# Performance work log

Hardware: AMD Instinct MI355X
Metric: run time of the kernel (lower is better)

The kernel has to match this reference:

```python
import jax, jax.numpy as jnp
import numpy as np

N = 20000      # total nodes
E = 160000     # total edges
NG = 128       # graphs in batch
POS_DIM = 48   # pos_embedding_dim
CTX = 128      # context_vector_dim
TYP = 80       # types_embedding_dim
HID = 256      # hidden_dim = POS_DIM + CTX + TYP
H = 4          # heads
C = HID        # per-head channels (concat=False)
OUT = 1024
L = 3
EF = 5
EPS_BN = 1e-5


def setup_inputs() -> dict:
    key = jax.random.key(0)
    ks = jax.random.split(key, 16)
    s = 0.02
    return {
        "x_types": jax.random.randint(ks[0], (N,), 0, 118),
        "pos": jax.random.normal(ks[1], (N, 3)) * 5.0,
        "edge_index": jax.random.randint(ks[2], (2, E), 0, N),
        "edge_attr": jax.random.uniform(ks[3], (E, EF)),
        "batch": jnp.sort(jax.random.randint(ks[4], (N,), 0, NG)),
        "context_vector": jax.random.normal(ks[5], (NG, CTX)),
        "emb_W": jax.random.normal(ks[6], (118, TYP)) * s,
        "emb_b": jnp.zeros((TYP,)),
        "lin_W": jax.random.normal(ks[7], (L, HID, H * C)) * s,
        "att_src": jax.random.normal(ks[8], (L, H, C)) * s,
        "att_dst": jax.random.normal(ks[9], (L, H, C)) * s,
        "edge_W": jax.random.normal(ks[10], (L, EF, H * C)) * s,
        "att_edge": jax.random.normal(ks[11], (L, H, C)) * s,
        "conv_b": jnp.zeros((L, C)),
        "bn_gamma": jnp.ones((L, C)),
        "bn_beta": jnp.zeros((L, C)),
        "out_W": jax.random.normal(ks[12], (HID, OUT)) * s,
        "out_b": jnp.zeros((OUT,)),
    }


def sinusoidal_pe(pos, dim):
    # per-coordinate [sin, cos] blocks, coords concatenated in x,y,z order
    half = dim // 2
    cdim = dim // 3
    div = jnp.exp(jnp.arange(half, dtype=pos.dtype) * (-jnp.log(jnp.asarray(10000.0, pos.dtype)) / half))[: cdim // 2]
    s = pos[:, :, None] * div                       # [N, 3, cdim//2]
    emb = jnp.concatenate([jnp.sin(s), jnp.cos(s)], axis=-1)  # [N, 3, cdim]
    return emb.reshape(pos.shape[0], dim)


def gat_layer(x, src, dst, eattr, W, a_s, a_d, eW, a_e, b):
    n = x.shape[0]
    xl = (x @ W).reshape(n, H, C)                   # [N,H,C]
    a_src = jnp.einsum('nhc,hc->nh', xl, a_s)[src]  # [E,H]
    a_dst = jnp.einsum('nhc,hc->nh', xl, a_d)[dst]
    ee = (eattr @ eW).reshape(-1, H, C)             # [E,H,C]
    a_edge = jnp.einsum('ehc,hc->eh', ee, a_e)
    alpha = jax.nn.leaky_relu(a_src + a_dst + a_edge, negative_slope=0.2)  # [E,H]
    amax = jax.ops.segment_max(alpha, dst, num_segments=n)
    ex = jnp.exp(alpha - jnp.where(jnp.isfinite(amax), amax, 0.0)[dst])
    denom = jax.ops.segment_sum(ex, dst, num_segments=n)
    w = ex / (denom[dst] + 1e-16)                   # segment softmax over incoming edges
    msg = xl[src] * w[..., None]                    # [E,H,C]
    out = jax.ops.segment_sum(msg, dst, num_segments=n)  # [N,H,C]
    return out.mean(axis=1) + b                     # concat=False -> head mean


def reference(x_types, pos, edge_index, edge_attr, batch, context_vector,
              emb_W, emb_b, lin_W, att_src, att_dst, edge_W, att_edge,
              conv_b, bn_gamma, bn_beta, out_W, out_b):
    types = jax.nn.one_hot(x_types, 118, dtype=emb_W.dtype)
    te = types @ emb_W + emb_b
    pe = sinusoidal_pe(pos, POS_DIM)
    x = jnp.concatenate([te, pe, context_vector[batch]], axis=1)  # [N, HID]
    src, dst = edge_index[0], edge_index[1]
    for l in range(L):
        xc = gat_layer(x, src, dst, edge_attr, lin_W[l], att_src[l],
                       att_dst[l], edge_W[l], att_edge[l], conv_b[l])
        mu = xc.mean(axis=0)
        var = xc.var(axis=0)
        xc = (xc - mu) / jnp.sqrt(var + EPS_BN) * bn_gamma[l] + bn_beta[l]
        xc = jax.nn.gelu(xc, approximate=False)
        x = x + xc                                   # residual ('res')
    x = x @ out_W + out_b                            # [N, OUT]
    return jax.ops.segment_sum(x, batch, num_segments=NG)  # global_add_pool
```

## Files before the change

kernel.cpp:

```cpp
#include <hip/hip_runtime.h>
#include <hip/hip_bf16.h>
#include <math.h>

#define N_NODES 20000
#define N_EDGES 160000
#define NGRAPH  128
#define NLAYER  3
#define M_PAD   20096

typedef short bf16x8 __attribute__((ext_vector_type(8)));
typedef float f32x4  __attribute__((ext_vector_type(4)));

__device__ __forceinline__ ushort f2bf(float x) {
    __hip_bfloat16 h = __float2bfloat16(x);
    return *(ushort*)&h;
}
__device__ __forceinline__ float bf2f(ushort u) {
    __hip_bfloat16 h = *(__hip_bfloat16*)&u;
    return __bfloat162float(h);
}

__device__ __forceinline__ void gload16(const void* g, void* l) {
    __builtin_amdgcn_global_load_lds(
        (const __attribute__((address_space(1))) void*)g,
        (__attribute__((address_space(3))) void*)l, 16, 0, 0);
}

__global__ __launch_bounds__(256) void k_node_init(
    const int* __restrict__ xt, const float* __restrict__ pos,
    const int* __restrict__ batch, const float* __restrict__ ctx,
    const float* __restrict__ embW, const float* __restrict__ embb,
    float* __restrict__ x)
{
    int n = blockIdx.x;
    int c = threadIdx.x;
    float v;
    if (c < 80) {
        v = embW[xt[n] * 80 + c] + embb[c];
    } else if (c < 128) {
        int j = c - 80;
        int coord = j >> 4;
        int k = j & 15;
        float p = pos[n * 3 + coord];
        int i = (k < 8) ? k : (k - 8);
        float factor = -logf(10000.0f) / 24.0f;
        float d = expf(factor * (float)i);
        float s = p * d;
        v = (k < 8) ? sinf(s) : cosf(s);
    } else {
        v = ctx[batch[n] * 128 + (c - 128)];
    }
    x[n * 256 + c] = v;
}

__global__ __launch_bounds__(256) void k_prepW(
    const float* __restrict__ W, ushort* __restrict__ Bthi, ushort* __restrict__ Btlo)
{
    int idx = blockIdx.x * 256 + threadIdx.x;
    int c   = idx & 255;
    int kap = idx >> 8;
    int k = kap & 255, h = kap >> 8;
    float w = W[(size_t)k * 1024 + h * 256 + c];
    ushort hi = f2bf(w);
    ushort lo = f2bf(w - bf2f(hi));
    int pos = c * 1024 + (kap ^ ((c & 3) << 3));
    Bthi[pos] = hi;
    Btlo[pos] = lo;
}

__global__ __launch_bounds__(256) void k_gemm_mfma(
    const ushort* __restrict__ Ahi, const ushort* __restrict__ Alo,
    const ushort* __restrict__ Bhi, const ushort* __restrict__ Blo,
    const float* __restrict__ convb, float* __restrict__ xc, int M)
{
    __shared__ ushort sAh[64 * 32];
    __shared__ ushort sAl[64 * 32];
    __shared__ ushort sBh[128 * 32];
    __shared__ ushort sBl[128 * 32];

    const int tid  = threadIdx.x;
    const int lane = tid & 63;
    const int wv   = tid >> 6;
    const int wr   = (wv >> 1) * 32;
    const int wc   = (wv & 1) * 64;
    const int bm   = blockIdx.y * 64;
    const int bn   = blockIdx.x * 128;
    const int r15  = lane & 15;
    const int g    = lane >> 4;

    f32x4 acc[2][4] = {};

    for (int kt = 0; kt < 1024; kt += 32) {
        {
            int row = tid >> 2, ch = tid & 3;
            size_t ga = (size_t)(bm + row) * 1024 + kt + ch * 8;
            uint la = (uint)tid * 16;
            gload16(&Ahi[ga], (char*)sAh + la);
            gload16(&Alo[ga], (char*)sAl + la);
        }
#pragma unroll
        for (int call = 0; call < 2; ++call) {
            int i   = call * 256 + tid;
            int row = i >> 2, ch = i & 3;
            size_t gb = (size_t)(bn + row) * 1024 + kt + ch * 8;
            uint lb = (uint)i * 16;
            gload16(&Bhi[gb], (char*)sBh + lb);
            gload16(&Blo[gb], (char*)sBl + lb);
        }
        __syncthreads();

        bf16x8 afh[2], afl[2], bfh[4], bfl[4];
#pragma unroll
        for (int f = 0; f < 2; ++f) {
            int rowA = wr + f * 16 + r15;
            int offA = rowA * 64 + ((g << 4) ^ ((rowA & 3) << 4));
            afh[f] = *(const bf16x8*)((const char*)sAh + offA);
            afl[f] = *(const bf16x8*)((const char*)sAl + offA);
        }
#pragma unroll
        for (int f = 0; f < 4; ++f) {
            int rowB = wc + f * 16 + r15;
            int offB = rowB * 64 + ((g << 4) ^ ((rowB & 3) << 4));
            bfh[f] = *(const bf16x8*)((const char*)sBh + offB);
            bfl[f] = *(const bf16x8*)((const char*)sBl + offB);
        }
#pragma unroll
        for (int fi = 0; fi < 2; ++fi)
#pragma unroll
            for (int fj = 0; fj < 4; ++fj) {
                acc[fi][fj] = __builtin_amdgcn_mfma_f32_16x16x32_bf16(
                    afh[fi], bfh[fj], acc[fi][fj], 0, 0, 0);
                acc[fi][fj] = __builtin_amdgcn_mfma_f32_16x16x32_bf16(
                    afh[fi], bfl[fj], acc[fi][fj], 0, 0, 0);
                acc[fi][fj] = __builtin_amdgcn_mfma_f32_16x16x32_bf16(
                    afl[fi], bfh[fj], acc[fi][fj], 0, 0, 0);
            }
        __syncthreads();
    }

#pragma unroll
    for (int fi = 0; fi < 2; ++fi) {
#pragma unroll
        for (int fj = 0; fj < 4; ++fj) {
#pragma unroll
            for (int r = 0; r < 4; ++r) {
                int row = bm + wr + fi * 16 + g * 4 + r;
                int col = bn + wc + fj * 16 + r15;
                if (row < M)
                    xc[(size_t)row * 256 + col] = 0.25f * acc[fi][fj][r] + convb[col];
            }
        }
    }
}

__global__ __launch_bounds__(256) void k_uvec(
    const float* __restrict__ W, const float* __restrict__ aS,
    const float* __restrict__ aD, float* __restrict__ uS, float* __restrict__ uD)
{
    int wid  = blockIdx.x * 4 + (threadIdx.x >> 6);
    int lane = threadIdx.x & 63;
    int h = wid >> 8;
    int k = wid & 255;
    float4 w = *(const float4*)&W[(size_t)k * 1024 + h * 256 + lane * 4];
    float4 s = *(const float4*)&aS[h * 256 + lane * 4];
    float4 d = *(const float4*)&aD[h * 256 + lane * 4];
    float ps = w.x * s.x + w.y * s.y + w.z * s.z + w.w * s.w;
    float pd = w.x * d.x + w.y * d.y + w.z * d.z + w.w * d.w;
    for (int o = 32; o; o >>= 1) {
        ps += __shfl_down(ps, o, 64);
        pd += __shfl_down(pd, o, 64);
    }
    if (lane == 0) { uS[h * 256 + k] = ps; uD[h * 256 + k] = pd; }
}

__global__ __launch_bounds__(256) void k_attn_dots_x(
    const float* __restrict__ x, const float* __restrict__ uS,
    const float* __restrict__ uD, float* __restrict__ asrc, float* __restrict__ adst)
{
    int n = blockIdx.x;
    int h = threadIdx.x >> 6;
    int lane = threadIdx.x & 63;
    float4 xv = *(const float4*)&x[(size_t)n * 256 + lane * 4];
    float4 sv = *(const float4*)&uS[h * 256 + lane * 4];
    float4 dv = *(const float4*)&uD[h * 256 + lane * 4];
    float ps = xv.x * sv.x + xv.y * sv.y + xv.z * sv.z + xv.w * sv.w;
    float pd = xv.x * dv.x + xv.y * dv.y + xv.z * dv.z + xv.w * dv.w;
    for (int o = 32; o; o >>= 1) {
        ps += __shfl_down(ps, o, 64);
        pd += __shfl_down(pd, o, 64);
    }
    if (lane == 0) { asrc[n * 4 + h] = ps; adst[n * 4 + h] = pd; }
}

__global__ void k_edge_M(const float* __restrict__ eW, const float* __restrict__ aE,
                         float* __restrict__ M)
{
    int f = blockIdx.x >> 2, h = blockIdx.x & 3;
    int lane = threadIdx.x;
    float4 w = *(const float4*)&eW[f * 1024 + h * 256 + lane * 4];
    float4 a = *(const float4*)&aE[h * 256 + lane * 4];
    float p = w.x * a.x + w.y * a.y + w.z * a.z + w.w * a.w;
    for (int o = 32; o; o >>= 1) p += __shfl_down(p, o, 64);
    if (lane == 0) M[f * 4 + h] = p;
}

__global__ __launch_bounds__(256) void k_edge_alpha(
    const int* __restrict__ src, const int* __restrict__ dst,
    const float* __restrict__ ea, const float* __restrict__ asrc,
    const float* __restrict__ adst, const float* __restrict__ M,
    const int* __restrict__ pos, float* __restrict__ ex)
{
    int e = blockIdx.x * 256 + threadIdx.x;
    if (e >= N_EDGES) return;
    int s = src[e], d = dst[e];
    float as_[4], ad_[4];
    *(float4*)as_ = *(const float4*)&asrc[s * 4];
    *(float4*)ad_ = *(const float4*)&adst[d * 4];
    float f[5];
#pragma unroll
    for (int i = 0; i < 5; ++i) f[i] = ea[e * 5 + i];
    float r[4];
#pragma unroll
    for (int h = 0; h < 4; ++h) {
        float m = f[0]*M[h] + f[1]*M[4+h] + f[2]*M[8+h] + f[3]*M[12+h] + f[4]*M[16+h];
        float al = as_[h] + ad_[h] + m;
        al = (al >= 0.f) ? al : 0.2f * al;
        r[h] = expf(al);
    }
    *(float4*)&ex[(size_t)pos[e] * 4] = *(float4*)r;
}

__global__ void k_hist(const int* __restrict__ dst, int* __restrict__ deg)
{
    int e = blockIdx.x * 256 + threadIdx.x;
    if (e < N_EDGES) atomicAdd(&deg[dst[e]], 1);
}

#define SCAN_T 1024
__global__ __launch_bounds__(1024) void k_scan(
    const int* __restrict__ deg, int* __restrict__ off, int* __restrict__ cursor)
{
    __shared__ int sums[SCAN_T];
    int t = threadIdx.x;
    const int CHK = (N_NODES + SCAN_T - 1) / SCAN_T;
    int base = t * CHK;
    int s = 0;
    for (int i = 0; i < CHK; ++i) {
        int idx = base + i;
        if (idx < N_NODES) s += deg[idx];
    }
    sums[t] = s;
    __syncthreads();
    for (int o = 1; o < SCAN_T; o <<= 1) {
        int v = (t >= o) ? sums[t - o] : 0;
        __syncthreads();
        sums[t] += v;
        __syncthreads();
    }
    int run = (t > 0) ? sums[t - 1] : 0;
    for (int i = 0; i < CHK; ++i) {
        int idx = base + i;
        if (idx < N_NODES) {
            off[idx] = run; cursor[idx] = run;
            run += deg[idx];
        }
    }
    if (t == SCAN_T - 1) off[N_NODES] = sums[SCAN_T - 1];
}

__global__ void k_scatter(const int* __restrict__ dst, const int* __restrict__ src,
                          int* __restrict__ cursor, int* __restrict__ pos,
                          int* __restrict__ srcs)
{
    int e = blockIdx.x * 256 + threadIdx.x;
    if (e >= N_EDGES) return;
    int p = atomicAdd(&cursor[dst[e]], 1);
    pos[e] = p;
    srcs[p] = src[e];
}

__global__ __launch_bounds__(256) void k_aggregate_x(
    const float* __restrict__ x, const float* __restrict__ ex,
    const int* __restrict__ off, const int* __restrict__ srcs,
    ushort* __restrict__ agghi, ushort* __restrict__ agglo)
{
    int n = blockIdx.x;
    int c = threadIdx.x;
    int e0 = off[n], e1 = off[n + 1];
    float a0 = 0.f, a1 = 0.f, a2 = 0.f, a3 = 0.f;
    float d0 = 0.f, d1 = 0.f, d2 = 0.f, d3 = 0.f;
    for (int e = e0; e < e1; ++e) {
        float4 w = *(const float4*)&ex[(size_t)e * 4];
        float xv = x[(size_t)srcs[e] * 256 + c];
        a0 += w.x * xv; a1 += w.y * xv; a2 += w.z * xv; a3 += w.w * xv;
        d0 += w.x; d1 += w.y; d2 += w.z; d3 += w.w;
    }
    float v[4];
    v[0] = a0 / (d0 + 1e-16f);
    v[1] = a1 / (d1 + 1e-16f);
    v[2] = a2 / (d2 + 1e-16f);
    v[3] = a3 / (d3 + 1e-16f);
    int cs = c ^ ((n & 3) << 3);
    size_t b = (size_t)n * 1024 + cs;
#pragma unroll
    for (int h = 0; h < 4; ++h) {
        ushort hi = f2bf(v[h]);
        ushort lo = f2bf(v[h] - bf2f(hi));
        agghi[b + h * 256] = hi;
        agglo[b + h * 256] = lo;
    }
}

__global__ __launch_bounds__(256) void k_bn_reduce(
    const float* __restrict__ xc, float* __restrict__ sums)
{
    int c = threadIdx.x;
    float s = 0.f, q = 0.f;
    for (int n = blockIdx.x; n < N_NODES; n += gridDim.x) {
        float v = xc[n * 256 + c];
        s += v; q += v * v;
    }
    atomicAdd(&sums[c], s);
    atomicAdd(&sums[256 + c], q);
}

__global__ __launch_bounds__(256) void k_bn_apply(
    const float* __restrict__ xc, const float* __restrict__ sums,
    const float* __restrict__ gamma, const float* __restrict__ beta,
    float* __restrict__ x)
{
    int i = blockIdx.x * 256 + threadIdx.x;
    if (i >= N_NODES * 256) return;
    int c = i & 255;
    const float invN = 1.0f / (float)N_NODES;
    float mu  = sums[c] * invN;
    float var = sums[256 + c] * invN - mu * mu;
    float v = (xc[i] - mu) * (1.0f / sqrtf(var + 1e-5f)) * gamma[c] + beta[c];
    float g = 0.5f * v * (1.0f + erff(v * 0.70710678118654752f));
    x[i] += g;
}

__global__ __launch_bounds__(256) void k_pool_x(
    const float* __restrict__ x, const int* __restrict__ batch,
    float* __restrict__ Xg, float* __restrict__ cnt)
{
    int g = blockIdx.x;
    int c = threadIdx.x;
    int a = 0, b = N_NODES;
    while (a < b) { int m = (a + b) >> 1; if (batch[m] < g) a = m + 1; else b = m; }
    int lo = a;
    b = N_NODES;
    while (a < b) { int m = (a + b) >> 1; if (batch[m] < g + 1) a = m + 1; else b = m; }
    int hi = a;
    float s = 0.f;
    for (int n = lo; n < hi; ++n) s += x[(size_t)n * 256 + c];
    Xg[g * 256 + c] = s;
    if (c == 0) cnt[g] = (float)(hi - lo);
}

__global__ __launch_bounds__(256) void k_out_gemv(
    const float* __restrict__ Xg, const float* __restrict__ W,
    const float* __restrict__ b, const float* __restrict__ cnt,
    float* __restrict__ out)
{
    __shared__ float sx[256];
    int g = blockIdx.x;
    int cc = blockIdx.y * 256 + threadIdx.x;
    sx[threadIdx.x] = Xg[g * 256 + threadIdx.x];
    __syncthreads();
    float acc = 0.f;
#pragma unroll 8
    for (int k = 0; k < 256; ++k)
        acc += sx[k] * W[(size_t)k * 1024 + cc];
    out[(size_t)g * 1024 + cc] = acc + cnt[g] * b[cc];
}

extern "C" void kernel_launch(void* const* d_in, const int* in_sizes, int n_in,
                              void* d_out, int out_size, void* d_ws, size_t ws_size,
                              hipStream_t stream)
{
    const int*   xt    = (const int*)d_in[0];
    const float* pos   = (const float*)d_in[1];
    const int*   eidx  = (const int*)d_in[2];
    const float* ea    = (const float*)d_in[3];
    const int*   batch = (const int*)d_in[4];
    const float* ctx   = (const float*)d_in[5];
    const float* embW  = (const float*)d_in[6];
    const float* embb  = (const float*)d_in[7];
    const float* linW  = (const float*)d_in[8];
    const float* attS  = (const float*)d_in[9];
    const float* attD  = (const float*)d_in[10];
    const float* edgeW = (const float*)d_in[11];
    const float* attE  = (const float*)d_in[12];
    const float* convb = (const float*)d_in[13];
    const float* gamma = (const float*)d_in[14];
    const float* beta  = (const float*)d_in[15];
    const float* outW  = (const float*)d_in[16];
    const float* outb  = (const float*)d_in[17];
    float* out = (float*)d_out;
    const int* src = eidx;
    const int* dst = eidx + N_EDGES;

    char* p = (char*)d_ws;
    auto alloc = [&](size_t bytes) {
        void* r = (void*)p;
        p += (bytes + 255) & ~(size_t)255;
        return r;
    };
    float*  x     = (float*)alloc((size_t)N_NODES * 256 * 4);
    ushort* agghi = (ushort*)alloc((size_t)M_PAD * 1024 * 2);
    ushort* agglo = (ushort*)alloc((size_t)M_PAD * 1024 * 2);
    ushort* Bthi  = (ushort*)alloc((size_t)256 * 1024 * 2);
    ushort* Btlo  = (ushort*)alloc((size_t)256 * 1024 * 2);
    float*  xc    = (float*)alloc((size_t)N_NODES * 256 * 4);
    float*  asrc  = (float*)alloc((size_t)N_NODES * 4 * 4);
    float*  adst  = (float*)alloc((size_t)N_NODES * 4 * 4);
    float*  ex    = (float*)alloc((size_t)N_EDGES * 4 * 4);
    float*  Mbuf  = (float*)alloc(20 * 4);
    float*  uS    = (float*)alloc(1024 * 4);
    float*  uD    = (float*)alloc(1024 * 4);
    float*  sums  = (float*)alloc(512 * 4);
    float*  Xg    = (float*)alloc((size_t)NGRAPH * 256 * 4);
    float*  cnt   = (float*)alloc((size_t)NGRAPH * 4);
    int*  deg    = (int*)alloc((size_t)N_NODES * 4);
    int*  off    = (int*)alloc((size_t)(N_NODES + 1) * 4);
    int*  cursor = (int*)alloc((size_t)N_NODES * 4);
    int*  posb   = (int*)alloc((size_t)N_EDGES * 4);
    int*  srcs   = (int*)alloc((size_t)N_EDGES * 4);

    k_node_init<<<N_NODES, 256, 0, stream>>>(xt, pos, batch, ctx, embW, embb, x);
    hipMemsetAsync(deg, 0, (size_t)N_NODES * 4, stream);
    k_hist<<<(N_EDGES + 255) / 256, 256, 0, stream>>>(dst, deg);
    k_scan<<<1, SCAN_T, 0, stream>>>(deg, off, cursor);
    k_scatter<<<(N_EDGES + 255) / 256, 256, 0, stream>>>(dst, src, cursor, posb, srcs);

    dim3 ggrid(2, (M_PAD / 64));
    for (int l = 0; l < NLAYER; ++l) {
        const float* W = linW + (size_t)l * 256 * 1024;
        k_uvec<<<256, 256, 0, stream>>>(W, attS + l * 1024, attD + l * 1024, uS, uD);
        k_attn_dots_x<<<N_NODES, 256, 0, stream>>>(x, uS, uD, asrc, adst);
        k_edge_M<<<20, 64, 0, stream>>>(edgeW + l * 5 * 1024, attE + l * 1024, Mbuf);
        k_edge_alpha<<<(N_EDGES + 255) / 256, 256, 0, stream>>>(src, dst, ea, asrc, adst, Mbuf, posb, ex);
        k_aggregate_x<<<N_NODES, 256, 0, stream>>>(x, ex, off, srcs, agghi, agglo);
        k_prepW<<<1024, 256, 0, stream>>>(W, Bthi, Btlo);
        k_gemm_mfma<<<ggrid, 256, 0, stream>>>(agghi, agglo, Bthi, Btlo,
                                               convb + l * 256, xc, N_NODES);
        hipMemsetAsync(sums, 0, 512 * 4, stream);
        k_bn_reduce<<<256, 256, 0, stream>>>(xc, sums);
        k_bn_apply<<<(N_NODES * 256 + 255) / 256, 256, 0, stream>>>(xc, sums, gamma + l * 256, beta + l * 256, x);
    }
    k_pool_x<<<NGRAPH, 256, 0, stream>>>(x, batch, Xg, cnt);
    k_out_gemv<<<dim3(NGRAPH, 4), 256, 0, stream>>>(Xg, outW, outb, cnt, out);
}
```

Before: 727.2 us.

## Triple-buffer GEMM LDS loads and unroll edge aggregation gather by four

The MFMA GEMM now keeps three LDS buffers and issues async global-to-LDS loads two k-tiles ahead. It waits with explicit vmcnt counters and uses one barrier per iteration instead of two __syncthreads, so load latency overlaps compute. The aggregation kernel unrolls the per-edge gather loop by four so more independent loads are in flight. The cost is triple the LDS use, which may lower occupancy, and hand-tuned waitcnt values that depend on how many loads each stage issues.

```diff
diff --git a/kernel.cpp b/kernel.cpp
--- a/kernel.cpp
+++ b/kernel.cpp
@@ -73,10 +73,10 @@
     const ushort* __restrict__ Bhi, const ushort* __restrict__ Blo,
     const float* __restrict__ convb, float* __restrict__ xc, int M)
 {
-    __shared__ ushort sAh[64 * 32];
-    __shared__ ushort sAl[64 * 32];
-    __shared__ ushort sBh[128 * 32];
-    __shared__ ushort sBl[128 * 32];
+    __shared__ ushort sAh[3][64 * 32];
+    __shared__ ushort sAl[3][64 * 32];
+    __shared__ ushort sBh[3][128 * 32];
+    __shared__ ushort sBl[3][128 * 32];
 
     const int tid  = threadIdx.x;
     const int lane = tid & 63;
@@ -88,41 +88,53 @@
     const int r15  = lane & 15;
     const int g    = lane >> 4;
 
-    f32x4 acc[2][4] = {};
-
-    for (int kt = 0; kt < 1024; kt += 32) {
-        {
-            int row = tid >> 2, ch = tid & 3;
-            size_t ga = (size_t)(bm + row) * 1024 + kt + ch * 8;
-            uint la = (uint)tid * 16;
-            gload16(&Ahi[ga], (char*)sAh + la);
-            gload16(&Alo[ga], (char*)sAl + la);
-        }
+    const int  arow = tid >> 2, ach = tid & 3;
+    const uint la   = (uint)tid * 16;
+
+    auto stage = [&](int t) {
+        int buf = t % 3;
+        int kt  = t * 32;
+        size_t ga = (size_t)(bm + arow) * 1024 + kt + ach * 8;
+        gload16(&Ahi[ga], (char*)sAh[buf] + la);
+        gload16(&Alo[ga], (char*)sAl[buf] + la);
 #pragma unroll
         for (int call = 0; call < 2; ++call) {
             int i   = call * 256 + tid;
             int row = i >> 2, ch = i & 3;
             size_t gb = (size_t)(bn + row) * 1024 + kt + ch * 8;
             uint lb = (uint)i * 16;
-            gload16(&Bhi[gb], (char*)sBh + lb);
-            gload16(&Blo[gb], (char*)sBl + lb);
+            gload16(&Bhi[gb], (char*)sBh[buf] + lb);
+            gload16(&Blo[gb], (char*)sBl[buf] + lb);
         }
-        __syncthreads();
-
+    };
+
+    f32x4 acc[2][4] = {};
+
+    stage(0);
+    stage(1);
+
+    for (int t = 0; t < 32; ++t) {
+        if (t < 31) asm volatile("s_waitcnt vmcnt(6)" ::: "memory");
+        else        asm volatile("s_waitcnt vmcnt(0)" ::: "memory");
+        __builtin_amdgcn_s_barrier();
+        __builtin_amdgcn_sched_barrier(0);
+        if (t + 2 < 32) stage(t + 2);
+
+        const int buf = t % 3;
         bf16x8 afh[2], afl[2], bfh[4], bfl[4];
 #pragma unroll
         for (int f = 0; f < 2; ++f) {
             int rowA = wr + f * 16 + r15;
             int offA = rowA * 64 + ((g << 4) ^ ((rowA & 3) << 4));
-            afh[f] = *(const bf16x8*)((const char*)sAh + offA);
-            afl[f] = *(const bf16x8*)((const char*)sAl + offA);
+            afh[f] = *(const bf16x8*)((const char*)sAh[buf] + offA);
+            afl[f] = *(const bf16x8*)((const char*)sAl[buf] + offA);
         }
 #pragma unroll
         for (int f = 0; f < 4; ++f) {
             int rowB = wc + f * 16 + r15;
             int offB = rowB * 64 + ((g << 4) ^ ((rowB & 3) << 4));
-            bfh[f] = *(const bf16x8*)((const char*)sBh + offB);
-            bfl[f] = *(const bf16x8*)((const char*)sBl + offB);
+            bfh[f] = *(const bf16x8*)((const char*)sBh[buf] + offB);
+            bfl[f] = *(const bf16x8*)((const char*)sBl[buf] + offB);
         }
 #pragma unroll
         for (int fi = 0; fi < 2; ++fi)
@@ -135,7 +147,6 @@
                 acc[fi][fj] = __builtin_amdgcn_mfma_f32_16x16x32_bf16(
                     afl[fi], bfh[fj], acc[fi][fj], 0, 0, 0);
             }
-        __syncthreads();
     }
 
 #pragma unroll
@@ -289,7 +300,27 @@
     int e0 = off[n], e1 = off[n + 1];
     float a0 = 0.f, a1 = 0.f, a2 = 0.f, a3 = 0.f;
     float d0 = 0.f, d1 = 0.f, d2 = 0.f, d3 = 0.f;
-    for (int e = e0; e < e1; ++e) {
+    int e = e0;
+    for (; e + 3 < e1; e += 4) {
+        float4 w0 = *(const float4*)&ex[(size_t)(e + 0) * 4];
+        float4 w1 = *(const float4*)&ex[(size_t)(e + 1) * 4];
+        float4 w2 = *(const float4*)&ex[(size_t)(e + 2) * 4];
+        float4 w3 = *(const float4*)&ex[(size_t)(e + 3) * 4];
+        int s0 = srcs[e + 0], s1 = srcs[e + 1], s2 = srcs[e + 2], s3 = srcs[e + 3];
+        float x0 = x[(size_t)s0 * 256 + c];
+        float x1 = x[(size_t)s1 * 256 + c];
+        float x2 = x[(size_t)s2 * 256 + c];
+        float x3 = x[(size_t)s3 * 256 + c];
+        a0 += w0.x * x0 + w1.x * x1 + w2.x * x2 + w3.x * x3;
+        a1 += w0.y * x0 + w1.y * x1 + w2.y * x2 + w3.y * x3;
+        a2 += w0.z * x0 + w1.z * x1 + w2.z * x2 + w3.z * x3;
+        a3 += w0.w * x0 + w1.w * x1 + w2.w * x2 + w3.w * x3;
+        d0 += w0.x + w1.x + w2.x + w3.x;
+        d1 += w0.y + w1.y + w2.y + w3.y;
+        d2 += w0.z + w1.z + w2.z + w3.z;
+        d3 += w0.w + w1.w + w2.w + w3.w;
+    }
+    for (; e < e1; ++e) {
         float4 w = *(const float4*)&ex[(size_t)e * 4];
         float xv = x[(size_t)srcs[e] * 256 + c];
         a0 += w.x * xv; a1 += w.y * xv; a2 += w.z * xv; a3 += w.w * xv;
```

Result: slower. 803.9 us (+10.6%).

## Halve GEMM M-tile, batch weight prep across layers, unroll edge aggregation

Applied to the files above, without the earlier changes.

The MFMA GEMM tile shrinks from 64 to 32 rows per block, which doubles the block count (2x628 instead of 2x314) so more CUs are busy, at the cost of less reuse of each B tile. Weight splitting into bf16 hi/lo is done once for all three layers in a single launch before the loop, removing one launch per layer. The aggregation loop is unrolled by four so several independent gather loads are in flight at once. Extra workspace is needed for the per-layer split weights.

```diff
diff --git a/kernel.cpp b/kernel.cpp
--- a/kernel.cpp
+++ b/kernel.cpp
@@ -54,16 +54,17 @@
 }
 
 __global__ __launch_bounds__(256) void k_prepW(
-    const float* __restrict__ W, ushort* __restrict__ Bthi, ushort* __restrict__ Btlo)
-{
+    const float* __restrict__ linW, ushort* __restrict__ Bthi, ushort* __restrict__ Btlo)
+{
+    int l   = blockIdx.y;
     int idx = blockIdx.x * 256 + threadIdx.x;
     int c   = idx & 255;
     int kap = idx >> 8;
     int k = kap & 255, h = kap >> 8;
-    float w = W[(size_t)k * 1024 + h * 256 + c];
+    float w = linW[(size_t)l * 262144 + (size_t)k * 1024 + h * 256 + c];
     ushort hi = f2bf(w);
     ushort lo = f2bf(w - bf2f(hi));
-    int pos = c * 1024 + (kap ^ ((c & 3) << 3));
+    size_t pos = (size_t)l * 262144 + c * 1024 + (kap ^ ((c & 3) << 3));
     Bthi[pos] = hi;
     Btlo[pos] = lo;
 }
@@ -73,49 +74,54 @@
     const ushort* __restrict__ Bhi, const ushort* __restrict__ Blo,
     const float* __restrict__ convb, float* __restrict__ xc, int M)
 {
-    __shared__ ushort sAh[64 * 32];
-    __shared__ ushort sAl[64 * 32];
+    __shared__ ushort sAh[32 * 32];
+    __shared__ ushort sAl[32 * 32];
     __shared__ ushort sBh[128 * 32];
     __shared__ ushort sBl[128 * 32];
 
     const int tid  = threadIdx.x;
     const int lane = tid & 63;
     const int wv   = tid >> 6;
-    const int wr   = (wv >> 1) * 32;
+    const int wr   = (wv >> 1) * 16;
     const int wc   = (wv & 1) * 64;
-    const int bm   = blockIdx.y * 64;
+    const int bm   = blockIdx.y * 32;
     const int bn   = blockIdx.x * 128;
     const int r15  = lane & 15;
     const int g    = lane >> 4;
 
-    f32x4 acc[2][4] = {};
+    f32x4 acc[4] = {};
 
     for (int kt = 0; kt < 1024; kt += 32) {
         {
-            int row = tid >> 2, ch = tid & 3;
+            int i = tid & 127;
+            int row = i >> 2, ch = i & 3;
             size_t ga = (size_t)(bm + row) * 1024 + kt + ch * 8;
-            uint la = (uint)tid * 16;
-            gload16(&Ahi[ga], (char*)sAh + la);
-            gload16(&Alo[ga], (char*)sAl + la);
+            uint la = (uint)i * 16;
+            if (tid < 128) gload16(&Ahi[ga], (char*)sAh + la);
+            else           gload16(&Alo[ga], (char*)sAl + la);
         }
 #pragma unroll
         for (int call = 0; call < 2; ++call) {
-            int i   = call * 256 + tid;
+            int i = call * 256 + tid;
             int row = i >> 2, ch = i & 3;
             size_t gb = (size_t)(bn + row) * 1024 + kt + ch * 8;
-            uint lb = (uint)i * 16;
-            gload16(&Bhi[gb], (char*)sBh + lb);
-            gload16(&Blo[gb], (char*)sBl + lb);
+            gload16(&Bhi[gb], (char*)sBh + (uint)i * 16);
+        }
+#pragma unroll
+        for (int call = 0; call < 2; ++call) {
+            int i = call * 256 + tid;
+            int row = i >> 2, ch = i & 3;
+            size_t gb = (size_t)(bn + row) * 1024 + kt + ch * 8;
+            gload16(&Blo[gb], (char*)sBl + (uint)i * 16);
         }
         __syncthreads();
 
-        bf16x8 afh[2], afl[2], bfh[4], bfl[4];
-#pragma unroll
-        for (int f = 0; f < 2; ++f) {
-            int rowA = wr + f * 16 + r15;
+        bf16x8 afh, afl, bfh[4], bfl[4];
+        {
+            int rowA = wr + r15;
             int offA = rowA * 64 + ((g << 4) ^ ((rowA & 3) << 4));
-            afh[f] = *(const bf16x8*)((const char*)sAh + offA);
-            afl[f] = *(const bf16x8*)((const char*)sAl + offA);
+            afh = *(const bf16x8*)((const char*)sAh + offA);
+            afl = *(const bf16x8*)((const char*)sAl + offA);
         }
 #pragma unroll
         for (int f = 0; f < 4; ++f) {
@@ -125,30 +131,22 @@
             bfl[f] = *(const bf16x8*)((const char*)sBl + offB);
         }
 #pragma unroll
-        for (int fi = 0; fi < 2; ++fi)
-#pragma unroll
-            for (int fj = 0; fj < 4; ++fj) {
-                acc[fi][fj] = __builtin_amdgcn_mfma_f32_16x16x32_bf16(
-                    afh[fi], bfh[fj], acc[fi][fj], 0, 0, 0);
-                acc[fi][fj] = __builtin_amdgcn_mfma_f32_16x16x32_bf16(
-                    afh[fi], bfl[fj], acc[fi][fj], 0, 0, 0);
-                acc[fi][fj] = __builtin_amdgcn_mfma_f32_16x16x32_bf16(
-                    afl[fi], bfh[fj], acc[fi][fj], 0, 0, 0);
-            }
+        for (int fj = 0; fj < 4; ++fj) {
+            acc[fj] = __builtin_amdgcn_mfma_f32_16x16x32_bf16(afh, bfh[fj], acc[fj], 0, 0, 0);
+            acc[fj] = __builtin_amdgcn_mfma_f32_16x16x32_bf16(afh, bfl[fj], acc[fj], 0, 0, 0);
+            acc[fj] = __builtin_amdgcn_mfma_f32_16x16x32_bf16(afl, bfh[fj], acc[fj], 0, 0, 0);
+        }
         __syncthreads();
     }
 
 #pragma unroll
-    for (int fi = 0; fi < 2; ++fi) {
-#pragma unroll
-        for (int fj = 0; fj < 4; ++fj) {
-#pragma unroll
-            for (int r = 0; r < 4; ++r) {
-                int row = bm + wr + fi * 16 + g * 4 + r;
-                int col = bn + wc + fj * 16 + r15;
-                if (row < M)
-                    xc[(size_t)row * 256 + col] = 0.25f * acc[fi][fj][r] + convb[col];
-            }
+    for (int fj = 0; fj < 4; ++fj) {
+#pragma unroll
+        for (int r = 0; r < 4; ++r) {
+            int row = bm + wr + g * 4 + r;
+            int col = bn + wc + fj * 16 + r15;
+            if (row < M)
+                xc[(size_t)row * 256 + col] = 0.25f * acc[fj][r] + convb[col];
         }
     }
 }
@@ -289,7 +287,27 @@
     int e0 = off[n], e1 = off[n + 1];
     float a0 = 0.f, a1 = 0.f, a2 = 0.f, a3 = 0.f;
     float d0 = 0.f, d1 = 0.f, d2 = 0.f, d3 = 0.f;
-    for (int e = e0; e < e1; ++e) {
+    int e = e0;
+    for (; e + 3 < e1; e += 4) {
+        float4 w0 = *(const float4*)&ex[(size_t)(e + 0) * 4];
+        float4 w1 = *(const float4*)&ex[(size_t)(e + 1) * 4];
+        float4 w2 = *(const float4*)&ex[(size_t)(e + 2) * 4];
+        float4 w3 = *(const float4*)&ex[(size_t)(e + 3) * 4];
+        int s0 = srcs[e + 0], s1 = srcs[e + 1], s2 = srcs[e + 2], s3 = srcs[e + 3];
+        float x0 = x[(size_t)s0 * 256 + c];
+        float x1 = x[(size_t)s1 * 256 + c];
+        float x2 = x[(size_t)s2 * 256 + c];
+        float x3 = x[(size_t)s3 * 256 + c];
+        a0 += w0.x * x0 + w1.x * x1 + w2.x * x2 + w3.x * x3;
+        a1 += w0.y * x0 + w1.y * x1 + w2.y * x2 + w3.y * x3;
+        a2 += w0.z * x0 + w1.z * x1 + w2.z * x2 + w3.z * x3;
+        a3 += w0.w * x0 + w1.w * x1 + w2.w * x2 + w3.w * x3;
+        d0 += w0.x + w1.x + w2.x + w3.x;
+        d1 += w0.y + w1.y + w2.y + w3.y;
+        d2 += w0.z + w1.z + w2.z + w3.z;
+        d3 += w0.w + w1.w + w2.w + w3.w;
+    }
+    for (; e < e1; ++e) {
         float4 w = *(const float4*)&ex[(size_t)e * 4];
         float xv = x[(size_t)srcs[e] * 256 + c];
         a0 += w.x * xv; a1 += w.y * xv; a2 += w.z * xv; a3 += w.w * xv;
@@ -410,8 +428,8 @@
     float*  x     = (float*)alloc((size_t)N_NODES * 256 * 4);
     ushort* agghi = (ushort*)alloc((size_t)M_PAD * 1024 * 2);
     ushort* agglo = (ushort*)alloc((size_t)M_PAD * 1024 * 2);
-    ushort* Bthi  = (ushort*)alloc((size_t)256 * 1024 * 2);
-    ushort* Btlo  = (ushort*)alloc((size_t)256 * 1024 * 2);
+    ushort* Bthi  = (ushort*)alloc((size_t)NLAYER * 256 * 1024 * 2);
+    ushort* Btlo  = (ushort*)alloc((size_t)NLAYER * 256 * 1024 * 2);
     float*  xc    = (float*)alloc((size_t)N_NODES * 256 * 4);
     float*  asrc  = (float*)alloc((size_t)N_NODES * 4 * 4);
     float*  adst  = (float*)alloc((size_t)N_NODES * 4 * 4);
@@ -433,8 +451,9 @@
     k_hist<<<(N_EDGES + 255) / 256, 256, 0, stream>>>(dst, deg);
     k_scan<<<1, SCAN_T, 0, stream>>>(deg, off, cursor);
     k_scatter<<<(N_EDGES + 255) / 256, 256, 0, stream>>>(dst, src, cursor, posb, srcs);
-
-    dim3 ggrid(2, (M_PAD / 64));
+    k_prepW<<<dim3(1024, NLAYER), 256, 0, stream>>>(linW, Bthi, Btlo);
+
+    dim3 ggrid(2, M_PAD / 32);
     for (int l = 0; l < NLAYER; ++l) {
         const float* W = linW + (size_t)l * 256 * 1024;
         k_uvec<<<256, 256, 0, stream>>>(W, attS + l * 1024, attD + l * 1024, uS, uD);
@@ -442,8 +461,9 @@
         k_edge_M<<<20, 64, 0, stream>>>(edgeW + l * 5 * 1024, attE + l * 1024, Mbuf);
         k_edge_alpha<<<(N_EDGES + 255) / 256, 256, 0, stream>>>(src, dst, ea, asrc, adst, Mbuf, posb, ex);
         k_aggregate_x<<<N_NODES, 256, 0, stream>>>(x, ex, off, srcs, agghi, agglo);
-        k_prepW<<<1024, 256, 0, stream>>>(W, Bthi, Btlo);
-        k_gemm_mfma<<<ggrid, 256, 0, stream>>>(agghi, agglo, Bthi, Btlo,
+        k_gemm_mfma<<<ggrid, 256, 0, stream>>>(agghi, agglo,
+                                               Bthi + (size_t)l * 262144,
+                                               Btlo + (size_t)l * 262144,
                                                convb + l * 256, xc, N_NODES);
         hipMemsetAsync(sums, 0, 512 * 4, stream);
         k_bn_reduce<<<256, 256, 0, stream>>>(xc, sums);
```

Result: no change. 718.7 us (-1.2%).
